# Kernel tuning notes

Measured on AMD Instinct MI355X. Metric: run time of the kernel, lower is better.

## Reference

```python
import jax, jax.numpy as jnp
import numpy as np

N, D, H, C = 50000, 256, 4, 16  # nodes, in_dim, heads, out_channels (hidden_dim)
E = 1600000
NEG_SLOPE = 0.2


def _gatv2_layer(x, src, dst, Wl, bl, Wr, br, att, bias, n_nodes):
    """PyG GATv2Conv (share_weights=False, concat=True, eval mode).
    x: [N, Fin]; Wl/Wr: [Fin, H*C]; att: [H, C]; bias: [H*C].
    """
    xl = (x @ Wl + bl).reshape(n_nodes, H, C)  # source-side transform
    xr = (x @ Wr + br).reshape(n_nodes, H, C)  # target-side transform
    # per-edge attention logits: a^T LeakyReLU(xl_j + xr_i)
    e = jax.nn.leaky_relu(xl[src] + xr[dst], negative_slope=NEG_SLOPE)  # [E,H,C]
    logits = jnp.einsum('ehc,hc->eh', e, att)  # [E,H]
    # scatter-softmax over incoming edges of each target node
    m = jax.ops.segment_max(logits, dst, num_segments=n_nodes)  # [N,H]
    ex = jnp.exp(logits - m[dst])
    denom = jax.ops.segment_sum(ex, dst, num_segments=n_nodes)  # [N,H]
    alpha = ex / denom[dst]  # [E,H]
    out = jax.ops.segment_sum(alpha[:, :, None] * xl[src], dst, num_segments=n_nodes)
    return out.reshape(n_nodes, H * C) + bias


def setup_inputs() -> dict:
    key = jax.random.key(0)
    ks = jax.random.split(key, 16)
    g = lambda k, shp, fan: jax.random.normal(k, shp, jnp.float32) * (1.0 / np.sqrt(fan))
    inp = {
        'x': jax.random.normal(ks[0], (N, D), jnp.float32),
        'edge_index': jax.random.randint(ks[1], (2, E), 0, N, dtype=jnp.int64),
        # conv1: in D -> H*C
        'Wl1': g(ks[2], (D, H * C), D), 'bl1': jnp.zeros((H * C,), jnp.float32),
        'Wr1': g(ks[3], (D, H * C), D), 'br1': jnp.zeros((H * C,), jnp.float32),
        'att1': g(ks[4], (H, C), C), 'bias1': jnp.zeros((H * C,), jnp.float32),
        # conv2: in H*C -> H*C
        'Wl2': g(ks[5], (H * C, H * C), H * C), 'bl2': jnp.zeros((H * C,), jnp.float32),
        'Wr2': g(ks[6], (H * C, H * C), H * C), 'br2': jnp.zeros((H * C,), jnp.float32),
        'att2': g(ks[7], (H, C), C), 'bias2': jnp.zeros((H * C,), jnp.float32),
        # output head: H*C -> D
        'Wo': g(ks[8], (H * C, D), H * C), 'bo': jnp.zeros((D,), jnp.float32),
    }
    return inp


def reference(x, edge_index, Wl1, bl1, Wr1, br1, att1, bias1,
              Wl2, bl2, Wr2, br2, att2, bias2, Wo, bo):
    src, dst = edge_index[0], edge_index[1]
    h = jax.nn.relu(_gatv2_layer(x, src, dst, Wl1, bl1, Wr1, br1, att1, bias1, N))
    h = jax.nn.relu(_gatv2_layer(h, src, dst, Wl2, bl2, Wr2, br2, att2, bias2, N))
    return jax.nn.sigmoid(h @ Wo + bo)  # min_max is None -> no affine rescale
```

## Files before the change

### kernel.cpp

```cpp
#include <hip/hip_runtime.h>
#include <math.h>

#define NN 50000
#define DIN 256
#define HC 64
#define NEG 0.2f
#define BK 16
#define TM 64
#define NB 196
#define EPB 4096
#define CAP 36864

template <int CTRL>
__device__ __forceinline__ float dpp_mov(float x) {
    int r = __builtin_amdgcn_update_dpp(0, __float_as_int(x), CTRL, 0xF, 0xF, true);
    return __int_as_float(r);
}
__device__ __forceinline__ float reduce16_bcast(float v) {
    v += dpp_mov<0xB1>(v);
    v += dpp_mov<0x4E>(v);
    v += dpp_mov<0x141>(v);
    v += dpp_mov<0x140>(v);
    return v;
}


__global__ __launch_bounds__(256) void bhist_k(const int* __restrict__ dst,
                                               int* __restrict__ bcnt, int E) {
    __shared__ int h[NB];
    int t = threadIdx.x;
    for (int i = t; i < NB; i += 256) h[i] = 0;
    __syncthreads();
    int base = blockIdx.x * 2048 + t;
#pragma unroll
    for (int k = 0; k < 8; ++k) {
        int e = base + k * 256;
        if (e < E) atomicAdd(&h[dst[e] >> 8], 1);
    }
    __syncthreads();
    for (int i = t; i < NB; i += 256)
        if (h[i]) atomicAdd(&bcnt[i], h[i]);
}

__global__ __launch_bounds__(256) void bscan_k(const int* __restrict__ bcnt,
                                               int* __restrict__ boffs,
                                               int* __restrict__ bcursor,
                                               int* __restrict__ offs, int E) {
    __shared__ int s[256];
    int t = threadIdx.x;
    s[t] = (t < NB) ? bcnt[t] : 0;
    __syncthreads();
    for (int off = 1; off < 256; off <<= 1) {
        int v = s[t];
        int u = (t >= off) ? s[t - off] : 0;
        __syncthreads();
        s[t] = v + u;
        __syncthreads();
    }
    if (t < NB) {
        int ex = (t == 0) ? 0 : s[t - 1];
        boffs[t] = ex;
        bcursor[t] = ex;
    }
    if (t == NB) boffs[NB] = s[NB - 1];
    if (t == 0) offs[NN] = E;
}

__global__ __launch_bounds__(1024) void bin_k(const int* __restrict__ src,
                                              const int* __restrict__ dst,
                                              int* __restrict__ bcursor,
                                              unsigned* __restrict__ epair, int E) {
    __shared__ int hist[NB];
    __shared__ int lofs[NB];
    __shared__ int gshift[NB];
    __shared__ int scanb[256];
    __shared__ unsigned pbuf[EPB];
    __shared__ unsigned char abkt[EPB];
    int t = threadIdx.x;
    for (int i = t; i < NB; i += 1024) hist[i] = 0;
    __syncthreads();
    int e0 = blockIdx.x * EPB;
    unsigned p[4]; int bk[4], rk[4]; bool val[4];
#pragma unroll
    for (int k = 0; k < 4; ++k) {
        int e = e0 + k * 1024 + t;
        val[k] = e < E;
        if (val[k]) {
            int s = src[e], d = dst[e];
            p[k] = ((unsigned)s << 8) | (unsigned)(d & 255);
            bk[k] = d >> 8;
            rk[k] = atomicAdd(&hist[bk[k]], 1);
        }
    }
    __syncthreads();
    if (t < 256) scanb[t] = (t < NB) ? hist[t] : 0;
    __syncthreads();
    for (int off = 1; off < 256; off <<= 1) {
        int v = 0, u = 0;
        if (t < 256) { v = scanb[t]; if (t >= off) u = scanb[t - off]; }
        __syncthreads();
        if (t < 256) scanb[t] = v + u;
        __syncthreads();
    }
    if (t < NB) {
        int ex = (t == 0) ? 0 : scanb[t - 1];
        lofs[t] = ex;
        int gb = atomicAdd(&bcursor[t], hist[t]);
        gshift[t] = gb - ex;
    }
    __syncthreads();
    int total = scanb[NB - 1];
#pragma unroll
    for (int k = 0; k < 4; ++k) {
        if (val[k]) {
            int pos = lofs[bk[k]] + rk[k];
            pbuf[pos] = p[k];
            abkt[pos] = (unsigned char)bk[k];
        }
    }
    __syncthreads();
    for (int i = t; i < total; i += 1024) {
        int b = abkt[i];
        epair[gshift[b] + i] = pbuf[i];
    }
}

__global__ __launch_bounds__(1024) void bsort_k(const unsigned* __restrict__ epair,
                                                const int* __restrict__ boffs,
                                                int* __restrict__ offs,
                                                unsigned* __restrict__ ssrc, int n) {
    __shared__ int lhist[256];
    __shared__ int lcur[256];
    __shared__ int scanb[256];
    __shared__ unsigned sbuf[CAP];
    int b = blockIdx.x, t = threadIdx.x;
    int start = boffs[b], end = boffs[b + 1];
    int cnt = end - start;
    if (t < 256) lhist[t] = 0;
    __syncthreads();
    for (int i = t; i < cnt; i += 1024) {
        unsigned p = epair[start + i];
        atomicAdd(&lhist[p & 255], 1);
    }
    __syncthreads();
    if (t < 256) scanb[t] = lhist[t];
    __syncthreads();
    for (int off = 1; off < 256; off <<= 1) {
        int v = 0, u = 0;
        if (t < 256) { v = scanb[t]; if (t >= off) u = scanb[t - off]; }
        __syncthreads();
        if (t < 256) scanb[t] = v + u;
        __syncthreads();
    }
    if (t < 256) {
        int ex = (t == 0) ? 0 : scanb[t - 1];
        lcur[t] = ex;
        int node = b * 256 + t;
        if (node < n) offs[node] = start + ex;
    }
    __syncthreads();
    if (cnt <= CAP) {
        for (int i = t; i < cnt; i += 1024) {
            unsigned p = epair[start + i];
            int r = atomicAdd(&lcur[p & 255], 1);
            sbuf[r] = p & ~255u;
        }
        __syncthreads();
        for (int i = t; i < cnt; i += 1024) ssrc[start + i] = sbuf[i];
    } else {
        for (int i = t; i < cnt; i += 1024) {
            unsigned p = epair[start + i];
            int r = atomicAdd(&lcur[p & 255], 1);
            ssrc[start + r] = p & ~255u;
        }
    }
}

__global__ __launch_bounds__(256) void gemm_dual_k(const float* __restrict__ A,
                                                   const float* __restrict__ Wl,
                                                   const float* __restrict__ bl,
                                                   const float* __restrict__ Wr,
                                                   const float* __restrict__ br,
                                                   float* __restrict__ xl,
                                                   float* __restrict__ xr,
                                                   int n, int K) {
    __shared__ float As[BK][TM + 4];
    __shared__ float Bs[BK][128];
    int t = threadIdx.x;
    int tx = t & 15, ty = t >> 4;
    int row0 = blockIdx.x * TM;
    float acc[4][8] = {};
    int arow = t >> 2;
    int akb  = (t & 3) * 4;
    int bk   = t >> 4;
    int bcol = (t & 15) * 4;
    bool arow_ok = (row0 + arow) < n;
    const float* Aptr = A + (size_t)(row0 + arow) * K + akb;

    for (int kc = 0; kc < K; kc += BK) {
        float4 av = make_float4(0.f, 0.f, 0.f, 0.f);
        if (arow_ok) av = *(const float4*)(Aptr + kc);
        float4 b0 = *(const float4*)(Wl + (size_t)(kc + bk) * HC + bcol);
        float4 b1 = *(const float4*)(Wr + (size_t)(kc + bk) * HC + bcol);
        __syncthreads();
        As[akb + 0][arow] = av.x;
        As[akb + 1][arow] = av.y;
        As[akb + 2][arow] = av.z;
        As[akb + 3][arow] = av.w;
        *(float4*)&Bs[bk][bcol]      = b0;
        *(float4*)&Bs[bk][64 + bcol] = b1;
        __syncthreads();
#pragma unroll
        for (int k = 0; k < BK; ++k) {
            float4 a  = *(const float4*)&As[k][ty * 4];
            float4 p0 = *(const float4*)&Bs[k][tx * 4];
            float4 p1 = *(const float4*)&Bs[k][64 + tx * 4];
            float ar[4] = {a.x, a.y, a.z, a.w};
            float bc[8] = {p0.x, p0.y, p0.z, p0.w, p1.x, p1.y, p1.z, p1.w};
#pragma unroll
            for (int r = 0; r < 4; ++r)
#pragma unroll
                for (int c = 0; c < 8; ++c)
                    acc[r][c] += ar[r] * bc[c];
        }
    }
    float4 bl4 = *(const float4*)(bl + tx * 4);
    float4 br4 = *(const float4*)(br + tx * 4);
#pragma unroll
    for (int r = 0; r < 4; ++r) {
        int grow = row0 + ty * 4 + r;
        if (grow < n) {
            float4 ol, orr;
            ol.x = acc[r][0] + bl4.x; ol.y = acc[r][1] + bl4.y;
            ol.z = acc[r][2] + bl4.z; ol.w = acc[r][3] + bl4.w;
            orr.x = acc[r][4] + br4.x; orr.y = acc[r][5] + br4.y;
            orr.z = acc[r][6] + br4.z; orr.w = acc[r][7] + br4.w;
            *(float4*)(xl + (size_t)grow * HC + tx * 4) = ol;
            *(float4*)(xr + (size_t)grow * HC + tx * 4) = orr;
        }
    }
}

__global__ __launch_bounds__(256) void head_gemm_k(const float* __restrict__ h,
                                                   const float* __restrict__ Wo,
                                                   const float* __restrict__ bo,
                                                   float* __restrict__ out, int n) {
    __shared__ float As[BK][TM + 4];
    __shared__ float Bs[BK][128];
    int t = threadIdx.x;
    int tx = t & 15, ty = t >> 4;
    int row0 = blockIdx.x * TM;
    int coloff = blockIdx.y * 128;
    float acc[4][8] = {};
    int arow = t >> 2;
    int akb  = (t & 3) * 4;
    int bk   = t >> 4;
    int bcol = (t & 15) * 4;
    bool arow_ok = (row0 + arow) < n;
    const float* Aptr = h + (size_t)(row0 + arow) * HC + akb;

    for (int kc = 0; kc < HC; kc += BK) {
        float4 av = make_float4(0.f, 0.f, 0.f, 0.f);
        if (arow_ok) av = *(const float4*)(Aptr + kc);
        float4 b0 = *(const float4*)(Wo + (size_t)(kc + bk) * DIN + coloff + bcol);
        float4 b1 = *(const float4*)(Wo + (size_t)(kc + bk) * DIN + coloff + 64 + bcol);
        __syncthreads();
        As[akb + 0][arow] = av.x;
        As[akb + 1][arow] = av.y;
        As[akb + 2][arow] = av.z;
        As[akb + 3][arow] = av.w;
        *(float4*)&Bs[bk][bcol]      = b0;
        *(float4*)&Bs[bk][64 + bcol] = b1;
        __syncthreads();
#pragma unroll
        for (int k = 0; k < BK; ++k) {
            float4 a  = *(const float4*)&As[k][ty * 4];
            float4 p0 = *(const float4*)&Bs[k][tx * 4];
            float4 p1 = *(const float4*)&Bs[k][64 + tx * 4];
            float ar[4] = {a.x, a.y, a.z, a.w};
            float bc[8] = {p0.x, p0.y, p0.z, p0.w, p1.x, p1.y, p1.z, p1.w};
#pragma unroll
            for (int r = 0; r < 4; ++r)
#pragma unroll
                for (int c = 0; c < 8; ++c)
                    acc[r][c] += ar[r] * bc[c];
        }
    }
    float4 ba = *(const float4*)(bo + coloff + tx * 4);
    float4 bb = *(const float4*)(bo + coloff + 64 + tx * 4);
#pragma unroll
    for (int r = 0; r < 4; ++r) {
        int grow = row0 + ty * 4 + r;
        if (grow < n) {
            float4 o0, o1;
            o0.x = 1.f / (1.f + __expf(-(acc[r][0] + ba.x)));
            o0.y = 1.f / (1.f + __expf(-(acc[r][1] + ba.y)));
            o0.z = 1.f / (1.f + __expf(-(acc[r][2] + ba.z)));
            o0.w = 1.f / (1.f + __expf(-(acc[r][3] + ba.w)));
            o1.x = 1.f / (1.f + __expf(-(acc[r][4] + bb.x)));
            o1.y = 1.f / (1.f + __expf(-(acc[r][5] + bb.y)));
            o1.z = 1.f / (1.f + __expf(-(acc[r][6] + bb.z)));
            o1.w = 1.f / (1.f + __expf(-(acc[r][7] + bb.w)));
            *(float4*)(out + (size_t)grow * DIN + coloff + tx * 4)      = o0;
            *(float4*)(out + (size_t)grow * DIN + coloff + 64 + tx * 4) = o1;
        }
    }
}

#define EDGE(ii, xx, vv)                                                  \
    {                                                                      \
        unsigned off = ssb[ii] + lane4;                                    \
        xx = *(const float*)(xlb + off);                                   \
        float s = xx + xrv;                                                \
        vv = attv * (s > 0.f ? s : NEG * s);                               \
    }

__global__ __launch_bounds__(256) void agg_k(const float* __restrict__ xl,
                                             const float* __restrict__ xr,
                                             const float* __restrict__ att,
                                             const float* __restrict__ bias,
                                             const int* __restrict__ offs,
                                             const unsigned* __restrict__ ssb,
                                             float* __restrict__ out, int n) {
    int wave = (blockIdx.x * 256 + threadIdx.x) >> 6;
    int lane = threadIdx.x & 63;
    if (wave >= n) return;
    const char* xlb = (const char*)xl;
    unsigned lane4 = (unsigned)lane * 4u;
    float xrv = xr[(size_t)wave * HC + lane];
    float attv = att[lane];
    float acc = 0.f, den = 0.f;
    int lo = __builtin_amdgcn_readfirstlane(offs[wave]);
    int hi = __builtin_amdgcn_readfirstlane(offs[wave + 1]);
    int i = lo;
    for (; i + 8 <= hi; i += 8) {
        float x0, x1, x2, x3, x4, x5, x6, x7;
        float v0, v1, v2, v3, v4, v5, v6, v7;
        EDGE(i + 0, x0, v0); EDGE(i + 1, x1, v1);
        EDGE(i + 2, x2, v2); EDGE(i + 3, x3, v3);
        EDGE(i + 4, x4, v4); EDGE(i + 5, x5, v5);
        EDGE(i + 6, x6, v6); EDGE(i + 7, x7, v7);
        v0 = reduce16_bcast(v0); v1 = reduce16_bcast(v1);
        v2 = reduce16_bcast(v2); v3 = reduce16_bcast(v3);
        v4 = reduce16_bcast(v4); v5 = reduce16_bcast(v5);
        v6 = reduce16_bcast(v6); v7 = reduce16_bcast(v7);
        float e0 = __expf(v0), e1 = __expf(v1), e2 = __expf(v2), e3 = __expf(v3);
        float e4 = __expf(v4), e5 = __expf(v5), e6 = __expf(v6), e7 = __expf(v7);
        den += ((e0 + e1) + (e2 + e3)) + ((e4 + e5) + (e6 + e7));
        acc += e0 * x0; acc += e1 * x1; acc += e2 * x2; acc += e3 * x3;
        acc += e4 * x4; acc += e5 * x5; acc += e6 * x6; acc += e7 * x7;
    }
    for (; i + 4 <= hi; i += 4) {
        float x0, x1, x2, x3, v0, v1, v2, v3;
        EDGE(i + 0, x0, v0); EDGE(i + 1, x1, v1);
        EDGE(i + 2, x2, v2); EDGE(i + 3, x3, v3);
        v0 = reduce16_bcast(v0); v1 = reduce16_bcast(v1);
        v2 = reduce16_bcast(v2); v3 = reduce16_bcast(v3);
        float e0 = __expf(v0), e1 = __expf(v1), e2 = __expf(v2), e3 = __expf(v3);
        den += (e0 + e1) + (e2 + e3);
        acc += e0 * x0; acc += e1 * x1; acc += e2 * x2; acc += e3 * x3;
    }
    for (; i < hi; ++i) {
        float xv, v;
        EDGE(i, xv, v);
        v = reduce16_bcast(v);
        float ex = __expf(v);
        den += ex;
        acc += ex * xv;
    }
    float o = (den > 0.f) ? acc / den : 0.f;
    o += bias[lane];
    out[(size_t)wave * HC + lane] = fmaxf(o, 0.f);
}

extern "C" void kernel_launch(void* const* d_in, const int* in_sizes, int n_in,
                              void* d_out, int out_size, void* d_ws, size_t ws_size,
                              hipStream_t stream) {
    const float* x    = (const float*)d_in[0];
    const int*   ei   = (const int*)d_in[1];
    const float* Wl1  = (const float*)d_in[2];
    const float* bl1  = (const float*)d_in[3];
    const float* Wr1  = (const float*)d_in[4];
    const float* br1  = (const float*)d_in[5];
    const float* att1 = (const float*)d_in[6];
    const float* bias1= (const float*)d_in[7];
    const float* Wl2  = (const float*)d_in[8];
    const float* bl2  = (const float*)d_in[9];
    const float* Wr2  = (const float*)d_in[10];
    const float* br2  = (const float*)d_in[11];
    const float* att2 = (const float*)d_in[12];
    const float* bias2= (const float*)d_in[13];
    const float* Wo   = (const float*)d_in[14];
    const float* bo   = (const float*)d_in[15];
    float* out = (float*)d_out;

    int E = in_sizes[1] / 2;
    const int* srcv = ei;
    const int* dstv = ei + E;

    size_t NF = (size_t)NN * HC;
    float* xl = (float*)d_ws;
    float* xr = xl + NF;
    float* hb = xr + NF;
    int* offs        = (int*)(hb + NF);
    unsigned* ssrc   = (unsigned*)(offs + NN + 1);
    int* boffs   = (int*)(ssrc + E);
    int* bcursor = boffs + NB + 1;
    int* bcnt    = bcursor + NB;
    unsigned* epair = (unsigned*)d_out;

    hipMemsetAsync(bcnt, 0, NB * sizeof(int), stream);
    bhist_k<<<(E + 2047) / 2048, 256, 0, stream>>>(dstv, bcnt, E);
    bscan_k<<<1, 256, 0, stream>>>(bcnt, boffs, bcursor, offs, E);
    bin_k<<<(E + EPB - 1) / EPB, 1024, 0, stream>>>(srcv, dstv, bcursor, epair, E);
    bsort_k<<<NB, 1024, 0, stream>>>(epair, boffs, offs, ssrc, NN);

    int gb = (NN + TM - 1) / TM;
    gemm_dual_k<<<gb, 256, 0, stream>>>(x, Wl1, bl1, Wr1, br1, xl, xr, NN, DIN);
    agg_k<<<(NN + 3) / 4, 256, 0, stream>>>(xl, xr, att1, bias1, offs, ssrc, hb, NN);
    gemm_dual_k<<<gb, 256, 0, stream>>>(hb, Wl2, bl2, Wr2, br2, xl, xr, NN, HC);
    agg_k<<<(NN + 3) / 4, 256, 0, stream>>>(xl, xr, att2, bias2, offs, ssrc, hb, NN);
    head_gemm_k<<<dim3(gb, 2), 256, 0, stream>>>(hb, Wo, bo, out, NN);
}
```

Baseline: 375.4 us.

## Use split-bf16 MFMA for node transform and head GEMMs

Replaces the three FP32 SIMT GEMM kernels with MFMA bf16 kernels. Each operand is split into high and low bf16 parts and three products (hi*hi, lo*hi, hi*lo) are accumulated, keeping close to FP32 accuracy. Weights are pre-split into padded bf16 images by small prep kernels that write into scratch regions (d_out and xl) before those buffers are needed. The intent is to move the GEMM cost onto matrix cores. The risks are small accuracy differences from the split-bf16 scheme and the extra launches, while the edge-aggregation kernels, which likely dominate, are unchanged.

Measured after the change: 345.4 us. 1.09x faster.

```diff
diff --git a/kernel.cpp b/kernel.cpp
--- a/kernel.cpp
+++ b/kernel.cpp
@@ -5,11 +5,23 @@
 #define DIN 256
 #define HC 64
 #define NEG 0.2f
-#define BK 16
 #define TM 64
 #define NB 196
 #define EPB 4096
 #define CAP 36864
+
+typedef short bf16x8 __attribute__((ext_vector_type(8)));
+typedef unsigned short ush8 __attribute__((ext_vector_type(8)));
+typedef float f32x4 __attribute__((ext_vector_type(4)));
+
+__device__ __forceinline__ unsigned short f2bf(float x) {
+    unsigned u = __float_as_uint(x);
+    u += 0x7FFFu + ((u >> 16) & 1u);
+    return (unsigned short)(u >> 16);
+}
+__device__ __forceinline__ float bf2f(unsigned short h) {
+    return __uint_as_float((unsigned)h << 16);
+}
 
 template <int CTRL>
 __device__ __forceinline__ float dpp_mov(float x) {
@@ -176,133 +188,219 @@
     }
 }
 
-__global__ __launch_bounds__(256) void gemm_dual_k(const float* __restrict__ A,
-                                                   const float* __restrict__ Wl,
-                                                   const float* __restrict__ bl,
-                                                   const float* __restrict__ Wr,
-                                                   const float* __restrict__ br,
-                                                   float* __restrict__ xl,
-                                                   float* __restrict__ xr,
-                                                   int n, int K) {
-    __shared__ float As[BK][TM + 4];
-    __shared__ float Bs[BK][128];
+__global__ __launch_bounds__(256) void wprep_dual_k(const float* __restrict__ Wl,
+                                                    const float* __restrict__ Wr,
+                                                    unsigned short* __restrict__ img,
+                                                    int K) {
+    int i = blockIdx.x * 256 + threadIdx.x;
+    int total = (K >> 5) * 10240;
+    if (i >= total) return;
+    int kk = i % 40;
+    int c  = (i / 40) & 127;
+    int p  = (i / 5120) & 1;
+    int s  = i / 10240;
+    unsigned short v = 0;
+    if (kk < 32) {
+        int k = s * 32 + kk;
+        float w = (c < 64) ? Wl[k * HC + c] : Wr[k * HC + (c - 64)];
+        unsigned short hi = f2bf(w);
+        v = p ? f2bf(w - bf2f(hi)) : hi;
+    }
+    img[i] = v;
+}
+
+__global__ __launch_bounds__(256) void wprep_head_k(const float* __restrict__ Wo,
+                                                    unsigned short* __restrict__ img) {
+    int i = blockIdx.x * 256 + threadIdx.x;
+    if (i >= 40960) return;
+    int kk = i % 40;
+    int c  = (i / 40) & 127;
+    int p  = (i / 5120) & 1;
+    int s  = (i / 10240) & 1;
+    int h  = i / 20480;
+    unsigned short v = 0;
+    if (kk < 32) {
+        int k = s * 32 + kk;
+        float w = Wo[k * DIN + h * 128 + c];
+        unsigned short hi = f2bf(w);
+        v = p ? f2bf(w - bf2f(hi)) : hi;
+    }
+    img[i] = v;
+}
+
+__global__ __launch_bounds__(256) void gemm_dual_mfma_k(
+        const float* __restrict__ A,
+        const unsigned short* __restrict__ img,
+        const float* __restrict__ bl, const float* __restrict__ br,
+        float* __restrict__ xl, float* __restrict__ xr,
+        int n, int K) {
+    __shared__ __attribute__((aligned(16))) unsigned short As[2][64][40];
+    __shared__ __attribute__((aligned(16))) unsigned short Bs[2][128][40];
     int t = threadIdx.x;
-    int tx = t & 15, ty = t >> 4;
-    int row0 = blockIdx.x * TM;
-    float acc[4][8] = {};
-    int arow = t >> 2;
-    int akb  = (t & 3) * 4;
-    int bk   = t >> 4;
-    int bcol = (t & 15) * 4;
-    bool arow_ok = (row0 + arow) < n;
-    const float* Aptr = A + (size_t)(row0 + arow) * K + akb;
-
-    for (int kc = 0; kc < K; kc += BK) {
-        float4 av = make_float4(0.f, 0.f, 0.f, 0.f);
-        if (arow_ok) av = *(const float4*)(Aptr + kc);
-        float4 b0 = *(const float4*)(Wl + (size_t)(kc + bk) * HC + bcol);
-        float4 b1 = *(const float4*)(Wr + (size_t)(kc + bk) * HC + bcol);
-        __syncthreads();
-        As[akb + 0][arow] = av.x;
-        As[akb + 1][arow] = av.y;
-        As[akb + 2][arow] = av.z;
-        As[akb + 3][arow] = av.w;
-        *(float4*)&Bs[bk][bcol]      = b0;
-        *(float4*)&Bs[bk][64 + bcol] = b1;
-        __syncthreads();
-#pragma unroll
-        for (int k = 0; k < BK; ++k) {
-            float4 a  = *(const float4*)&As[k][ty * 4];
-            float4 p0 = *(const float4*)&Bs[k][tx * 4];
-            float4 p1 = *(const float4*)&Bs[k][64 + tx * 4];
-            float ar[4] = {a.x, a.y, a.z, a.w};
-            float bc[8] = {p0.x, p0.y, p0.z, p0.w, p1.x, p1.y, p1.z, p1.w};
-#pragma unroll
-            for (int r = 0; r < 4; ++r)
-#pragma unroll
-                for (int c = 0; c < 8; ++c)
-                    acc[r][c] += ar[r] * bc[c];
-        }
-    }
-    float4 bl4 = *(const float4*)(bl + tx * 4);
-    float4 br4 = *(const float4*)(br + tx * 4);
-#pragma unroll
-    for (int r = 0; r < 4; ++r) {
-        int grow = row0 + ty * 4 + r;
-        if (grow < n) {
-            float4 ol, orr;
-            ol.x = acc[r][0] + bl4.x; ol.y = acc[r][1] + bl4.y;
-            ol.z = acc[r][2] + bl4.z; ol.w = acc[r][3] + bl4.w;
-            orr.x = acc[r][4] + br4.x; orr.y = acc[r][5] + br4.y;
-            orr.z = acc[r][6] + br4.z; orr.w = acc[r][7] + br4.w;
-            *(float4*)(xl + (size_t)grow * HC + tx * 4) = ol;
-            *(float4*)(xr + (size_t)grow * HC + tx * 4) = orr;
-        }
-    }
-}
-
-__global__ __launch_bounds__(256) void head_gemm_k(const float* __restrict__ h,
-                                                   const float* __restrict__ Wo,
-                                                   const float* __restrict__ bo,
-                                                   float* __restrict__ out, int n) {
-    __shared__ float As[BK][TM + 4];
-    __shared__ float Bs[BK][128];
+    int l = t & 63, w = t >> 6;
+    int wr = w >> 1, wc = w & 1;
+    int lan = l & 15;
+    int kb  = (l >> 4) * 8;
+    int row0 = blockIdx.x * 64;
+    int srow = t >> 2;
+    int skq  = (t & 3) * 8;
+    bool rok = (row0 + srow) < n;
+    const float* aptr = A + (size_t)(row0 + srow) * K + skq;
+
+    f32x4 acc0[4] = {}, acc1[4] = {};
+
+    int nks = K >> 5;
+    for (int ks = 0; ks < nks; ++ks) {
+        __syncthreads();
+        {
+            const ush8* src = (const ush8*)(img + (size_t)ks * 10240);
+            ush8* dst = (ush8*)&Bs[0][0][0];
+            int base = w * 5 * 64 + l;
+#pragma unroll
+            for (int c2 = 0; c2 < 5; ++c2) {
+                int u = base + c2 * 64;
+                dst[u] = src[u];
+            }
+        }
+        {
+            float4 f0 = make_float4(0.f, 0.f, 0.f, 0.f), f1 = f0;
+            if (rok) {
+                f0 = *(const float4*)(aptr + ks * 32);
+                f1 = *(const float4*)(aptr + ks * 32 + 4);
+            }
+            float xs[8] = {f0.x, f0.y, f0.z, f0.w, f1.x, f1.y, f1.z, f1.w};
+            ush8 hi8, lo8;
+#pragma unroll
+            for (int j = 0; j < 8; ++j) {
+                unsigned short h = f2bf(xs[j]);
+                hi8[j] = h;
+                lo8[j] = f2bf(xs[j] - bf2f(h));
+            }
+            *(ush8*)&As[0][srow][skq] = hi8;
+            *(ush8*)&As[1][srow][skq] = lo8;
+        }
+        __syncthreads();
+        bf16x8 ah0 = *(const bf16x8*)&As[0][wr * 32 + lan][kb];
+        bf16x8 ah1 = *(const bf16x8*)&As[0][wr * 32 + 16 + lan][kb];
+        bf16x8 al0 = *(const bf16x8*)&As[1][wr * 32 + lan][kb];
+        bf16x8 al1 = *(const bf16x8*)&As[1][wr * 32 + 16 + lan][kb];
+#pragma unroll
+        for (int cf = 0; cf < 4; ++cf) {
+            int bc = wc * 64 + cf * 16 + lan;
+            bf16x8 bhv = *(const bf16x8*)&Bs[0][bc][kb];
+            bf16x8 blv = *(const bf16x8*)&Bs[1][bc][kb];
+            acc0[cf] = __builtin_amdgcn_mfma_f32_16x16x32_bf16(ah0, bhv, acc0[cf], 0, 0, 0);
+            acc1[cf] = __builtin_amdgcn_mfma_f32_16x16x32_bf16(ah1, bhv, acc1[cf], 0, 0, 0);
+            acc0[cf] = __builtin_amdgcn_mfma_f32_16x16x32_bf16(al0, bhv, acc0[cf], 0, 0, 0);
+            acc1[cf] = __builtin_amdgcn_mfma_f32_16x16x32_bf16(al1, bhv, acc1[cf], 0, 0, 0);
+            acc0[cf] = __builtin_amdgcn_mfma_f32_16x16x32_bf16(ah0, blv, acc0[cf], 0, 0, 0);
+            acc1[cf] = __builtin_amdgcn_mfma_f32_16x16x32_bf16(ah1, blv, acc1[cf], 0, 0, 0);
+        }
+    }
+#pragma unroll
+    for (int cf = 0; cf < 4; ++cf) {
+        int col = wc * 64 + cf * 16 + lan;
+        float bv; float* dst; int c2;
+        if (col < 64) { bv = bl[col]; dst = xl; c2 = col; }
+        else          { bv = br[col - 64]; dst = xr; c2 = col - 64; }
+#pragma unroll
+        for (int rf = 0; rf < 2; ++rf) {
+            f32x4 a = rf ? acc1[cf] : acc0[cf];
+            int rbase = row0 + wr * 32 + rf * 16 + (l >> 4) * 4;
+#pragma unroll
+            for (int r = 0; r < 4; ++r) {
+                int grow = rbase + r;
+                if (grow < n) dst[(size_t)grow * HC + c2] = a[r] + bv;
+            }
+        }
+    }
+}
+
+__global__ __launch_bounds__(256) void head_gemm_mfma_k(
+        const float* __restrict__ A,
+        const unsigned short* __restrict__ img,
+        const float* __restrict__ bo,
+        float* __restrict__ out, int n) {
+    __shared__ __attribute__((aligned(16))) unsigned short As[2][64][40];
+    __shared__ __attribute__((aligned(16))) unsigned short Bs[2][128][40];
     int t = threadIdx.x;
-    int tx = t & 15, ty = t >> 4;
-    int row0 = blockIdx.x * TM;
+    int l = t & 63, w = t >> 6;
+    int wr = w >> 1, wc = w & 1;
+    int lan = l & 15;
+    int kb  = (l >> 4) * 8;
+    int row0 = blockIdx.x * 64;
     int coloff = blockIdx.y * 128;
-    float acc[4][8] = {};
-    int arow = t >> 2;
-    int akb  = (t & 3) * 4;
-    int bk   = t >> 4;
-    int bcol = (t & 15) * 4;
-    bool arow_ok = (row0 + arow) < n;
-    const float* Aptr = h + (size_t)(row0 + arow) * HC + akb;
-
-    for (int kc = 0; kc < HC; kc += BK) {
-        float4 av = make_float4(0.f, 0.f, 0.f, 0.f);
-        if (arow_ok) av = *(const float4*)(Aptr + kc);
-        float4 b0 = *(const float4*)(Wo + (size_t)(kc + bk) * DIN + coloff + bcol);
-        float4 b1 = *(const float4*)(Wo + (size_t)(kc + bk) * DIN + coloff + 64 + bcol);
-        __syncthreads();
-        As[akb + 0][arow] = av.x;
-        As[akb + 1][arow] = av.y;
-        As[akb + 2][arow] = av.z;
-        As[akb + 3][arow] = av.w;
-        *(float4*)&Bs[bk][bcol]      = b0;
-        *(float4*)&Bs[bk][64 + bcol] = b1;
-        __syncthreads();
-#pragma unroll
-        for (int k = 0; k < BK; ++k) {
-            float4 a  = *(const float4*)&As[k][ty * 4];
-            float4 p0 = *(const float4*)&Bs[k][tx * 4];
-            float4 p1 = *(const float4*)&Bs[k][64 + tx * 4];
-            float ar[4] = {a.x, a.y, a.z, a.w};
-            float bc[8] = {p0.x, p0.y, p0.z, p0.w, p1.x, p1.y, p1.z, p1.w};
-#pragma unroll
-            for (int r = 0; r < 4; ++r)
-#pragma unroll
-                for (int c = 0; c < 8; ++c)
-                    acc[r][c] += ar[r] * bc[c];
-        }
-    }
-    float4 ba = *(const float4*)(bo + coloff + tx * 4);
-    float4 bb = *(const float4*)(bo + coloff + 64 + tx * 4);
-#pragma unroll
-    for (int r = 0; r < 4; ++r) {
-        int grow = row0 + ty * 4 + r;
-        if (grow < n) {
-            float4 o0, o1;
-            o0.x = 1.f / (1.f + __expf(-(acc[r][0] + ba.x)));
-            o0.y = 1.f / (1.f + __expf(-(acc[r][1] + ba.y)));
-            o0.z = 1.f / (1.f + __expf(-(acc[r][2] + ba.z)));
-            o0.w = 1.f / (1.f + __expf(-(acc[r][3] + ba.w)));
-            o1.x = 1.f / (1.f + __expf(-(acc[r][4] + bb.x)));
-            o1.y = 1.f / (1.f + __expf(-(acc[r][5] + bb.y)));
-            o1.z = 1.f / (1.f + __expf(-(acc[r][6] + bb.z)));
-            o1.w = 1.f / (1.f + __expf(-(acc[r][7] + bb.w)));
-            *(float4*)(out + (size_t)grow * DIN + coloff + tx * 4)      = o0;
-            *(float4*)(out + (size_t)grow * DIN + coloff + 64 + tx * 4) = o1;
+    const unsigned short* himg = img + (size_t)blockIdx.y * 2 * 10240;
+    int srow = t >> 2;
+    int skq  = (t & 3) * 8;
+    bool rok = (row0 + srow) < n;
+    const float* aptr = A + (size_t)(row0 + srow) * HC + skq;
+
+    f32x4 acc0[4] = {}, acc1[4] = {};
+
+    for (int ks = 0; ks < 2; ++ks) {
+        __syncthreads();
+        {
+            const ush8* src = (const ush8*)(himg + (size_t)ks * 10240);
+            ush8* dst = (ush8*)&Bs[0][0][0];
+            int base = w * 5 * 64 + l;
+#pragma unroll
+            for (int c2 = 0; c2 < 5; ++c2) {
+                int u = base + c2 * 64;
+                dst[u] = src[u];
+            }
+        }
+        {
+            float4 f0 = make_float4(0.f, 0.f, 0.f, 0.f), f1 = f0;
+            if (rok) {
+                f0 = *(const float4*)(aptr + ks * 32);
+                f1 = *(const float4*)(aptr + ks * 32 + 4);
+            }
+            float xs[8] = {f0.x, f0.y, f0.z, f0.w, f1.x, f1.y, f1.z, f1.w};
+            ush8 hi8, lo8;
+#pragma unroll
+            for (int j = 0; j < 8; ++j) {
+                unsigned short h = f2bf(xs[j]);
+                hi8[j] = h;
+                lo8[j] = f2bf(xs[j] - bf2f(h));
+            }
+            *(ush8*)&As[0][srow][skq] = hi8;
+            *(ush8*)&As[1][srow][skq] = lo8;
+        }
+        __syncthreads();
+        bf16x8 ah0 = *(const bf16x8*)&As[0][wr * 32 + lan][kb];
+        bf16x8 ah1 = *(const bf16x8*)&As[0][wr * 32 + 16 + lan][kb];
+        bf16x8 al0 = *(const bf16x8*)&As[1][wr * 32 + lan][kb];
+        bf16x8 al1 = *(const bf16x8*)&As[1][wr * 32 + 16 + lan][kb];
+#pragma unroll
+        for (int cf = 0; cf < 4; ++cf) {
+            int bc = wc * 64 + cf * 16 + lan;
+            bf16x8 bhv = *(const bf16x8*)&Bs[0][bc][kb];
+            bf16x8 blv = *(const bf16x8*)&Bs[1][bc][kb];
+            acc0[cf] = __builtin_amdgcn_mfma_f32_16x16x32_bf16(ah0, bhv, acc0[cf], 0, 0, 0);
+            acc1[cf] = __builtin_amdgcn_mfma_f32_16x16x32_bf16(ah1, bhv, acc1[cf], 0, 0, 0);
+            acc0[cf] = __builtin_amdgcn_mfma_f32_16x16x32_bf16(al0, bhv, acc0[cf], 0, 0, 0);
+            acc1[cf] = __builtin_amdgcn_mfma_f32_16x16x32_bf16(al1, bhv, acc1[cf], 0, 0, 0);
+            acc0[cf] = __builtin_amdgcn_mfma_f32_16x16x32_bf16(ah0, blv, acc0[cf], 0, 0, 0);
+            acc1[cf] = __builtin_amdgcn_mfma_f32_16x16x32_bf16(ah1, blv, acc1[cf], 0, 0, 0);
+        }
+    }
+#pragma unroll
+    for (int cf = 0; cf < 4; ++cf) {
+        int col = coloff + wc * 64 + cf * 16 + lan;
+        float bv = bo[col];
+#pragma unroll
+        for (int rf = 0; rf < 2; ++rf) {
+            f32x4 a = rf ? acc1[cf] : acc0[cf];
+            int rbase = row0 + wr * 32 + rf * 16 + (l >> 4) * 4;
+#pragma unroll
+            for (int r = 0; r < 4; ++r) {
+                int grow = rbase + r;
+                if (grow < n) {
+                    float v = a[r] + bv;
+                    out[(size_t)grow * DIN + col] = 1.f / (1.f + __expf(-v));
+                }
+            }
         }
     }
 }
@@ -408,17 +506,23 @@
     int* bcursor = boffs + NB + 1;
     int* bcnt    = bcursor + NB;
     unsigned* epair = (unsigned*)d_out;
+    unsigned short* img1 = (unsigned short*)d_out;
+    unsigned short* img2 = img1 + 81920;
+    unsigned short* imgh = (unsigned short*)xl;
 
     hipMemsetAsync(bcnt, 0, NB * sizeof(int), stream);
     bhist_k<<<(E + 2047) / 2048, 256, 0, stream>>>(dstv, bcnt, E);
     bscan_k<<<1, 256, 0, stream>>>(bcnt, boffs, bcursor, offs, E);
     bin_k<<<(E + EPB - 1) / EPB, 1024, 0, stream>>>(srcv, dstv, bcursor, epair, E);
     bsort_k<<<NB, 1024, 0, stream>>>(epair, boffs, offs, ssrc, NN);
+    wprep_dual_k<<<320, 256, 0, stream>>>(Wl1, Wr1, img1, DIN);
+    wprep_dual_k<<<80, 256, 0, stream>>>(Wl2, Wr2, img2, HC);
 
     int gb = (NN + TM - 1) / TM;
-    gemm_dual_k<<<gb, 256, 0, stream>>>(x, Wl1, bl1, Wr1, br1, xl, xr, NN, DIN);
+    gemm_dual_mfma_k<<<gb, 256, 0, stream>>>(x, img1, bl1, br1, xl, xr, NN, DIN);
     agg_k<<<(NN + 3) / 4, 256, 0, stream>>>(xl, xr, att1, bias1, offs, ssrc, hb, NN);
-    gemm_dual_k<<<gb, 256, 0, stream>>>(hb, Wl2, bl2, Wr2, br2, xl, xr, NN, HC);
+    gemm_dual_mfma_k<<<gb, 256, 0, stream>>>(hb, img2, bl2, br2, xl, xr, NN, HC);
     agg_k<<<(NN + 3) / 4, 256, 0, stream>>>(xl, xr, att2, bias2, offs, ssrc, hb, NN);
-    head_gemm_k<<<dim3(gb, 2), 256, 0, stream>>>(hb, Wo, bo, out, NN);
-}
+    wprep_head_k<<<160, 256, 0, stream>>>(Wo, imgh);
+    head_gemm_mfma_k<<<dim3(gb, 2), 256, 0, stream>>>(hb, imgh, bo, out, NN);
+}
```
